# Kernel optimization log

Hardware: AMD Instinct MI355X
Metric: run time of the kernel (lower is better)

## Reference

```python
import jax, jax.numpy as jnp
import numpy as np

N = 4096
C = 64
B = 4
DIST_THRESHOLD = 0.5
ALPHA = 0.01
NEG_INF = -1e15


def setup_inputs() -> dict:
    key = jax.random.key(0)
    k1, k2, k3, k4, k5 = jax.random.split(key, 5)
    x = jax.random.normal(k1, (B, N, C), dtype=jnp.float32)
    dist_mat = jax.random.uniform(k2, (N, N), dtype=jnp.float32)
    proj_w = jax.random.normal(k3, (N, C, C), dtype=jnp.float32) / np.sqrt(C)
    proj_b = jax.random.normal(k4, (N, C), dtype=jnp.float32) * 0.01
    a_w = jax.random.normal(k5, (N, 2 * C), dtype=jnp.float32) / np.sqrt(2 * C)
    return {"x": x, "dist_mat": dist_mat, "proj_w": proj_w, "proj_b": proj_b, "a_w": a_w}


def reference(x, dist_mat, proj_w, proj_b, a_w):
    # Adjacency: (0 < dist < threshold), diagonal forced to 1.
    adj = (dist_mat > 0) & (dist_mat < DIST_THRESHOLD)
    adj = adj | jnp.eye(N, dtype=bool)

    # Per-node projection (GraphDense): h[b,n,:] = x[b,n,:] @ proj_w[n] + proj_b[n]
    h = jnp.einsum('bnc,nco->bno', x, proj_w) + proj_b  # [B, N, C]

    # Attention score: a[j] . concat(h_i, h_j) without materializing [B,N,N,2C].
    a_src, a_dst = a_w[:, :C], a_w[:, C:]               # each [N, C]
    s = jnp.einsum('bic,jc->bij', h, a_src) + jnp.einsum('bjc,jc->bj', h, a_dst)[:, None, :]
    s = jnp.where(s >= 0, s, ALPHA * s)                 # LeakyReLU
    s = jnp.where(adj[None, :, :], s, NEG_INF)          # mask non-edges
    att = jax.nn.softmax(s, axis=-1)                    # [B, N, N]

    # Weighted aggregation over neighbors.
    y = jnp.einsum('bij,bjc->bic', att, h)              # [B, N, C]
    return y
```

## Files before the change

kernel.cpp:

```cpp
#include <hip/hip_runtime.h>

#define N 4096
#define C 64
#define B 4
#define SHIFT 12.0f
#define CH 256

typedef __attribute__((ext_vector_type(8))) short short8;
typedef __attribute__((ext_vector_type(4))) short s16x4;
typedef __attribute__((ext_vector_type(4))) float f32x4;
typedef unsigned long long u64;

#define MFMA16(a, b, c) __builtin_amdgcn_mfma_f32_16x16x32_bf16(a, b, c, 0, 0, 0)

__device__ __forceinline__ short f2bf(float f) {
    unsigned u = __builtin_bit_cast(unsigned, f);
    u += 0x7fffu + ((u >> 16) & 1u);
    return (short)(u >> 16);
}

__global__ __launch_bounds__(256) void mask_kernel(const float* __restrict__ dist,
                                                   u64* __restrict__ msk) {
    const int wave = threadIdx.x >> 6, lane = threadIdx.x & 63;
    const int i = blockIdx.x * 4 + wave;
    const float* row = dist + (size_t)i * N;
#pragma unroll 8
    for (int jb = 0; jb < N / 64; jb++) {
        float d = row[jb * 64 + lane];
        u64 m = __ballot(d > 0.f && d < 0.5f);
        int dj = i - jb * 64;
        if (dj >= 0 && dj < 64) m |= (1ull << dj);
        if (lane == 0) msk[(size_t)i * (N / 64) + jb] = m;
    }
}

__global__ __launch_bounds__(256) void proj_kernel(
    const float* __restrict__ x,
    const float* __restrict__ proj_w,
    const float* __restrict__ proj_b,
    const float* __restrict__ a_w,
    short* __restrict__ h_bf,
    short* __restrict__ a_srcb,
    float* __restrict__ e2)
{
    __shared__ float lds_x[4][B][C];

    const int tid = threadIdx.x;
    const int wave = tid >> 6;
    const int lane = tid & 63;
    const int g = lane >> 4;
    const int o4 = lane & 15;
    const int n = blockIdx.x * 4 + wave;
    const float* Wn = proj_w + (size_t)n * C * C;

#pragma unroll
    for (int b = 0; b < B; b++)
        lds_x[wave][b][lane] = x[((size_t)b * N + n) * C + lane];

    float4 wbuf[16];
#pragma unroll
    for (int p = 0; p < 16; p++)
        wbuf[p] = *(const float4*)(Wn + (p * 4 + g) * C + o4 * 4);

    float acc[B][4];
#pragma unroll
    for (int b = 0; b < B; b++)
#pragma unroll
        for (int r = 0; r < 4; r++) acc[b][r] = 0.f;

#pragma unroll
    for (int p = 0; p < 16; p++) {
        float xs[B];
#pragma unroll
        for (int b = 0; b < B; b++) xs[b] = lds_x[wave][b][p * 4 + g];
#pragma unroll
        for (int b = 0; b < B; b++) {
            acc[b][0] = fmaf(xs[b], wbuf[p].x, acc[b][0]);
            acc[b][1] = fmaf(xs[b], wbuf[p].y, acc[b][1]);
            acc[b][2] = fmaf(xs[b], wbuf[p].z, acc[b][2]);
            acc[b][3] = fmaf(xs[b], wbuf[p].w, acc[b][3]);
        }
    }

#pragma unroll
    for (int b = 0; b < B; b++)
#pragma unroll
        for (int r = 0; r < 4; r++) {
            acc[b][r] += __shfl_xor(acc[b][r], 16, 64);
            acc[b][r] += __shfl_xor(acc[b][r], 32, 64);
        }

    float4 pb4 = *(const float4*)(proj_b + (size_t)n * C + o4 * 4);
#pragma unroll
    for (int b = 0; b < B; b++) {
        acc[b][0] += pb4.x; acc[b][1] += pb4.y;
        acc[b][2] += pb4.z; acc[b][3] += pb4.w;
    }

    float hg[4];
#pragma unroll
    for (int r = 0; r < 4; r++) {
        float v01 = (g & 1) ? acc[1][r] : acc[0][r];
        float v23 = (g & 1) ? acc[3][r] : acc[2][r];
        hg[r] = (g & 2) ? v23 : v01;
    }

    {
        s16x4 hv;
#pragma unroll
        for (int r = 0; r < 4; r++) hv[r] = f2bf(hg[r]);
        *(s16x4*)&h_bf[((size_t)g * N + n) * C + o4 * 4] = hv;
    }

    if (g == 0) {
        float4 as4 = *(const float4*)(a_w + (size_t)n * 2 * C + o4 * 4);
        s16x4 av;
        av[0] = f2bf(as4.x); av[1] = f2bf(as4.y);
        av[2] = f2bf(as4.z); av[3] = f2bf(as4.w);
        *(s16x4*)&a_srcb[(size_t)n * C + o4 * 4] = av;
    }

    {
        float4 ad4 = *(const float4*)(a_w + (size_t)n * 2 * C + C + o4 * 4);
        float s = hg[0] * ad4.x + hg[1] * ad4.y + hg[2] * ad4.z + hg[3] * ad4.w;
        s += __shfl_xor(s, 1, 64);
        s += __shfl_xor(s, 2, 64);
        s += __shfl_xor(s, 4, 64);
        s += __shfl_xor(s, 8, 64);
        if (o4 == 0) e2[g * N + n] = s - SHIFT;
    }
}

__global__ __launch_bounds__(256) void transpose_kernel(const short* __restrict__ h_bf,
                                                        short* __restrict__ hT_bf) {
    __shared__ short tile[64][72];
    const int t = threadIdx.x;
    const int b = blockIdx.y;
    const int n0 = blockIdx.x * 64;
    {
        int r = t >> 2, cs = (t & 3) * 16;
        const short* src = h_bf + ((size_t)b * N + n0 + r) * C + cs;
#pragma unroll
        for (int q = 0; q < 4; q++)
            *(s16x4*)&tile[r][cs + q * 4] = *(const s16x4*)(src + q * 4);
    }
    __syncthreads();
    {
        int c = t >> 2, ns = (t & 3) * 16;
        short v[16];
#pragma unroll
        for (int k = 0; k < 16; k++) v[k] = tile[ns + k][c];
        short* dst = hT_bf + (size_t)b * C * N + (size_t)c * N + n0 + ns;
        *(short8*)dst = *(short8*)&v[0];
        *(short8*)(dst + 8) = *(short8*)&v[8];
    }
}

__global__ __launch_bounds__(256) void attn_kernel(
    const u64* __restrict__ msk,
    const short* __restrict__ h_bf,
    const short* __restrict__ hT_bf,
    const short* __restrict__ a_srcb,
    const float* __restrict__ e2,
    float* __restrict__ part_y,
    float* __restrict__ part_l,
    int JS, int S, int mode)
{
    __shared__ short lds_a[CH][72];

    const int tid = threadIdx.x;
    const int wave = tid >> 6;
    const int lane = tid & 63;
    const int cl = lane & 15;
    const int rg = lane >> 4;
    const int rg8 = rg * 8;
    const int b = wave;
    const int sy = blockIdx.x % S;
    const int ix = blockIdx.x / S;
    const int i0 = ix * 32;
    const int jbeg = sy * JS;

    short8 bfr[2][2];
#pragma unroll
    for (int u = 0; u < 2; u++) {
        const short* hrow = h_bf + ((size_t)b * N + i0 + u * 16 + cl) * C;
        bfr[u][0] = *(const short8*)(hrow + rg8);
        bfr[u][1] = *(const short8*)(hrow + 32 + rg8);
    }

    const u64* mr0 = msk + (size_t)(i0 + cl) * (N / 64);
    const u64* mr1 = msk + (size_t)(i0 + 16 + cl) * (N / 64);

    f32x4 yacc[2][4];
#pragma unroll
    for (int u = 0; u < 2; u++)
#pragma unroll
        for (int t = 0; t < 4; t++) { f32x4 z = {0.f, 0.f, 0.f, 0.f}; yacc[u][t] = z; }
    f32x4 yl[2];
    { f32x4 z = {0.f, 0.f, 0.f, 0.f}; yl[0] = z; yl[1] = z; }

    short8 ones;
#pragma unroll
    for (int k = 0; k < 8; k++) ones[k] = (short)0x3F80;

    const float* eb = e2 + (size_t)b * N;
    const short* hp[4];
#pragma unroll
    for (int t = 0; t < 4; t++)
        hp[t] = hT_bf + (size_t)b * C * N + (size_t)(t * 16 + cl) * N + jbeg + rg8;

    const int jr = ((cl >> 2) << 3) | (cl & 3);

    for (int c0 = jbeg; c0 < jbeg + JS; c0 += CH) {
        __syncthreads();
#pragma unroll 8
        for (int q = 0; q < 8; q++) {
            int idx = q * 256 + tid;
            int row = idx >> 3, col = (idx & 7) * 8;
            *(short8*)&lds_a[row][col] =
                *(const short8*)(a_srcb + (size_t)c0 * 64 + idx * 8);
        }
        __syncthreads();

        for (int j0 = c0; j0 < c0 + CH; j0 += 64) {
            const int jl = j0 - c0;
            const u64 mbs0 = mr0[j0 >> 6], mbs1 = mr1[j0 >> 6];

            short8 pa[2][2];
#pragma unroll
            for (int u = 0; u < 2; u++) {
                const u64 mb = u ? mbs1 : mbs0;
                f32x4 st[4];
#pragma unroll
                for (int t = 0; t < 4; t++) {
                    const int tq = t >> 1, tr = t & 1;
                    const int vrow = jl + jr + tq * 32 + tr * 4;
                    short8 a0 = *(const short8*)&lds_a[vrow][rg8];
                    short8 a1 = *(const short8*)&lds_a[vrow][32 + rg8];
                    f32x4 eq = *(const f32x4*)(eb + j0 + tq * 32 + tr * 4 + rg8);
                    unsigned w32 = tq ? (unsigned)(mb >> 32) : (unsigned)mb;
                    unsigned ws = w32 >> (rg8 + tr * 4);
                    f32x4 z;
#pragma unroll
                    for (int r = 0; r < 4; r++)
                        z[r] = ((ws >> r) & 1u) ? eq[r] : -1e30f;
                    z = MFMA16(a0, bfr[u][0], z);
                    z = MFMA16(a1, bfr[u][1], z);
                    st[t] = z;
                }

                short8 q0, q1;
#pragma unroll
                for (int t = 0; t < 4; t++) {
#pragma unroll
                    for (int r = 0; r < 4; r++) {
                        float sv = st[t][r];
                        float pv = __expf(fmaxf(sv, fmaf(0.01f, sv, -11.88f)));
                        short bv = f2bf(pv);
                        if (t < 2) q0[(t & 1) * 4 + r] = bv;
                        else       q1[(t & 1) * 4 + r] = bv;
                    }
                }
                pa[u][0] = q0;
                pa[u][1] = q1;

                yl[u] = MFMA16(pa[u][0], ones, yl[u]);
                yl[u] = MFMA16(pa[u][1], ones, yl[u]);
            }

#pragma unroll
            for (int t = 0; t < 4; t++) {
                short8 h0 = *(const short8*)(hp[t]);
                short8 h1 = *(const short8*)(hp[t] + 32);
                yacc[0][t] = MFMA16(pa[0][0], h0, yacc[0][t]);
                yacc[0][t] = MFMA16(pa[0][1], h1, yacc[0][t]);
                yacc[1][t] = MFMA16(pa[1][0], h0, yacc[1][t]);
                yacc[1][t] = MFMA16(pa[1][1], h1, yacc[1][t]);
                hp[t] += 64;
            }
        }
    }

    if (mode) {
#pragma unroll
        for (int u = 0; u < 2; u++) {
            f32x4 inv;
#pragma unroll
            for (int r = 0; r < 4; r++) inv[r] = 1.f / yl[u][r];
#pragma unroll
            for (int t = 0; t < 4; t++)
#pragma unroll
                for (int r = 0; r < 4; r++)
                    part_y[((size_t)b * N + i0 + u * 16 + rg * 4 + r) * C + t * 16 + cl] =
                        yacc[u][t][r] * inv[r];
        }
    } else {
        size_t sb = (size_t)(sy * B + b) * N;
#pragma unroll
        for (int u = 0; u < 2; u++) {
#pragma unroll
            for (int t = 0; t < 4; t++)
#pragma unroll
                for (int r = 0; r < 4; r++)
                    part_y[(sb + i0 + u * 16 + rg * 4 + r) * C + t * 16 + cl] = yacc[u][t][r];
            if (cl == 0) *(f32x4*)&part_l[sb + i0 + u * 16 + rg * 4] = yl[u];
        }
    }
}

__global__ __launch_bounds__(256) void combine_kernel(
    const float* __restrict__ part_y, const float* __restrict__ part_l,
    float* __restrict__ out, int S)
{
    int g = blockIdx.x * 256 + threadIdx.x;
    int c4 = (g & 15) * 4;
    int row = (g >> 4) & (N - 1);
    int b = g >> 16;
    int bn = b * N + row;
    f32x4 y = {0.f, 0.f, 0.f, 0.f};
    float l = 0.f;
    if (S == 8) {
#pragma unroll
        for (int s = 0; s < 8; s++) {
            l += part_l[s * (B * N) + bn];
            f32x4 v = *(const f32x4*)&part_y[((size_t)s * B * N + bn) * C + c4];
#pragma unroll
            for (int r = 0; r < 4; r++) y[r] += v[r];
        }
    } else {
        for (int s = 0; s < S; s++) {
            l += part_l[s * (B * N) + bn];
            f32x4 v = *(const f32x4*)&part_y[((size_t)s * B * N + bn) * C + c4];
#pragma unroll
            for (int r = 0; r < 4; r++) y[r] += v[r];
        }
    }
    float inv = 1.f / l;
    f32x4 o;
#pragma unroll
    for (int r = 0; r < 4; r++) o[r] = y[r] * inv;
    *(f32x4*)&out[(size_t)g * 4] = o;
}

extern "C" void kernel_launch(void* const* d_in, const int* in_sizes, int n_in,
                              void* d_out, int out_size, void* d_ws, size_t ws_size,
                              hipStream_t stream) {
    const float* x      = (const float*)d_in[0];
    const float* dist   = (const float*)d_in[1];
    const float* proj_w = (const float*)d_in[2];
    const float* proj_b = (const float*)d_in[3];
    const float* a_w    = (const float*)d_in[4];
    float* out = (float*)d_out;

    char* ws = (char*)d_ws;
    short* h_bf   = (short*)(ws);
    short* hT_bf  = (short*)(ws + (2u << 20));
    short* a_srcb = (short*)(ws + (4u << 20));
    float* e2     = (float*)(ws + (4u << 20) + (512u << 10));
    u64*   msk    = (u64*)  (ws + (5u << 20));
    float* part_l = (float*)(ws + (7u << 20));
    float* part_y = (float*)(ws + (8u << 20));

    proj_kernel<<<N / 4, 256, 0, stream>>>(x, proj_w, proj_b, a_w, h_bf, a_srcb, e2);
    transpose_kernel<<<dim3(N / 64, B), 256, 0, stream>>>(h_bf, hT_bf);
    mask_kernel<<<N / 4, 256, 0, stream>>>(dist, msk);

    int S = 8;
    while (S > 1 && (8u << 20) + (size_t)S * B * N * C * 4 > ws_size) S >>= 1;
    bool direct = ((8u << 20) + (size_t)B * N * C * 4 > ws_size);

    if (direct) {
        attn_kernel<<<N / 32, 256, 0, stream>>>(
            msk, h_bf, hT_bf, a_srcb, e2, out, part_l, N, 1, 1);
    } else {
        attn_kernel<<<(N / 32) * S, 256, 0, stream>>>(
            msk, h_bf, hT_bf, a_srcb, e2, part_y, part_l, N / S, S, 0);
        combine_kernel<<<(B * N * C / 4) / 256, 256, 0, stream>>>(part_y, part_l, out, S);
    }
}
```

Baseline: 258.2 us.

## Fuse mask build and h transpose into projection kernel

Folds the adjacency bitmask construction and the transposed bf16 copy of h into the projection kernel, removing two separate kernel launches. Each block now streams four rows of dist_mat alongside its projection weights and writes hT directly from LDS. This cuts launch overhead and the reread of h_bf, but the transposed stores are narrow 8-byte writes strided by N, which may coalesce poorly.

```diff
diff --git a/kernel.cpp b/kernel.cpp
--- a/kernel.cpp
+++ b/kernel.cpp
@@ -19,31 +19,20 @@
     return (short)(u >> 16);
 }
 
-__global__ __launch_bounds__(256) void mask_kernel(const float* __restrict__ dist,
-                                                   u64* __restrict__ msk) {
-    const int wave = threadIdx.x >> 6, lane = threadIdx.x & 63;
-    const int i = blockIdx.x * 4 + wave;
-    const float* row = dist + (size_t)i * N;
-#pragma unroll 8
-    for (int jb = 0; jb < N / 64; jb++) {
-        float d = row[jb * 64 + lane];
-        u64 m = __ballot(d > 0.f && d < 0.5f);
-        int dj = i - jb * 64;
-        if (dj >= 0 && dj < 64) m |= (1ull << dj);
-        if (lane == 0) msk[(size_t)i * (N / 64) + jb] = m;
-    }
-}
-
 __global__ __launch_bounds__(256) void proj_kernel(
     const float* __restrict__ x,
+    const float* __restrict__ dist,
     const float* __restrict__ proj_w,
     const float* __restrict__ proj_b,
     const float* __restrict__ a_w,
     short* __restrict__ h_bf,
+    short* __restrict__ hT_bf,
     short* __restrict__ a_srcb,
-    float* __restrict__ e2)
+    float* __restrict__ e2,
+    u64* __restrict__ msk)
 {
     __shared__ float lds_x[4][B][C];
+    __shared__ short lds_h[B][4][C];
 
     const int tid = threadIdx.x;
     const int wave = tid >> 6;
@@ -62,6 +51,18 @@
     for (int p = 0; p < 16; p++)
         wbuf[p] = *(const float4*)(Wn + (p * 4 + g) * C + o4 * 4);
 
+    {
+        const float* drow = dist + (size_t)n * N;
+#pragma unroll 8
+        for (int jb = 0; jb < N / 64; jb++) {
+            float d = drow[jb * 64 + lane];
+            u64 m = __ballot(d > 0.f && d < 0.5f);
+            int dj = n - jb * 64;
+            if (dj >= 0 && dj < 64) m |= (1ull << dj);
+            if (lane == 0) msk[(size_t)n * (N / 64) + jb] = m;
+        }
+    }
+
     float acc[B][4];
 #pragma unroll
     for (int b = 0; b < B; b++)
@@ -110,6 +111,7 @@
 #pragma unroll
         for (int r = 0; r < 4; r++) hv[r] = f2bf(hg[r]);
         *(s16x4*)&h_bf[((size_t)g * N + n) * C + o4 * 4] = hv;
+        *(s16x4*)&lds_h[g][wave][o4 * 4] = hv;
     }
 
     if (g == 0) {
@@ -129,30 +131,14 @@
         s += __shfl_xor(s, 8, 64);
         if (o4 == 0) e2[g * N + n] = s - SHIFT;
     }
-}
-
-__global__ __launch_bounds__(256) void transpose_kernel(const short* __restrict__ h_bf,
-                                                        short* __restrict__ hT_bf) {
-    __shared__ short tile[64][72];
-    const int t = threadIdx.x;
-    const int b = blockIdx.y;
-    const int n0 = blockIdx.x * 64;
-    {
-        int r = t >> 2, cs = (t & 3) * 16;
-        const short* src = h_bf + ((size_t)b * N + n0 + r) * C + cs;
-#pragma unroll
-        for (int q = 0; q < 4; q++)
-            *(s16x4*)&tile[r][cs + q * 4] = *(const s16x4*)(src + q * 4);
-    }
+
     __syncthreads();
     {
-        int c = t >> 2, ns = (t & 3) * 16;
-        short v[16];
-#pragma unroll
-        for (int k = 0; k < 16; k++) v[k] = tile[ns + k][c];
-        short* dst = hT_bf + (size_t)b * C * N + (size_t)c * N + n0 + ns;
-        *(short8*)dst = *(short8*)&v[0];
-        *(short8*)(dst + 8) = *(short8*)&v[8];
+        const int b = wave, c = lane;
+        s16x4 v;
+#pragma unroll
+        for (int k = 0; k < 4; k++) v[k] = lds_h[b][k][c];
+        *(s16x4*)&hT_bf[(size_t)b * C * N + (size_t)c * N + blockIdx.x * 4] = v;
     }
 }
 
@@ -361,9 +347,8 @@
     float* part_l = (float*)(ws + (7u << 20));
     float* part_y = (float*)(ws + (8u << 20));
 
-    proj_kernel<<<N / 4, 256, 0, stream>>>(x, proj_w, proj_b, a_w, h_bf, a_srcb, e2);
-    transpose_kernel<<<dim3(N / 64, B), 256, 0, stream>>>(h_bf, hT_bf);
-    mask_kernel<<<N / 4, 256, 0, stream>>>(dist, msk);
+    proj_kernel<<<N / 4, 256, 0, stream>>>(x, dist, proj_w, proj_b, a_w,
+                                           h_bf, hT_bf, a_srcb, e2, msk);
 
     int S = 8;
     while (S > 1 && (8u << 20) + (size_t)S * B * N * C * 4 > ws_size) S >>= 1;
```

Result: no change. 253.8 us (-1.7%).
